# Optimization experiments

Measured on AMD Instinct MI355X. Metric: run time of the kernel, lower is better.

Reference implementation:

```python
import jax, jax.numpy as jnp
import numpy as np

N, E, F, H, DE, C, G = 50000, 800000, 128, 128, 16, 2, 32
NEG_SLOPE = 0.2

def setup_inputs() -> dict:
    key = jax.random.key(0)
    ks = jax.random.split(key, 13)
    s = 0.05  # small init scale for weights
    return {
        "x": jax.random.normal(ks[0], (N, F), jnp.float32),
        "edge_index": jax.random.randint(ks[1], (2, E), 0, N, dtype=jnp.int32),
        "edge_attr": jax.random.normal(ks[2], (E, DE), jnp.float32),
        "batch": jnp.sort(jax.random.randint(ks[3], (N,), 0, G, dtype=jnp.int32)),
        "Wl": jax.random.normal(ks[4], (F, H), jnp.float32) * s,
        "bl": jnp.zeros((H,), jnp.float32),
        "Wr": jax.random.normal(ks[5], (F, H), jnp.float32) * s,
        "br": jnp.zeros((H,), jnp.float32),
        "We": jax.random.normal(ks[6], (DE, H), jnp.float32) * s,
        "att": jax.random.normal(ks[7], (H,), jnp.float32) * s,
        "bias_conv": jnp.zeros((H,), jnp.float32),
        "Wc": jax.random.normal(ks[8], (H, C), jnp.float32) * s,
        "bc": jnp.zeros((C,), jnp.float32),
    }

def reference(x, edge_index, edge_attr, batch, Wl, bl, Wr, br, We, att, bias_conv, Wc, bc):
    n = x.shape[0]
    src, dst = edge_index[0], edge_index[1]
    # add self loops; self-loop edge_attr = mean of incoming edge_attr (PyG fill_value='mean')
    ones_e = jnp.ones((edge_attr.shape[0],), x.dtype)
    deg = jax.ops.segment_sum(ones_e, dst, num_segments=n)
    loop_attr = jax.ops.segment_sum(edge_attr, dst, num_segments=n) / jnp.maximum(deg, 1.0)[:, None]
    idx = jnp.arange(n, dtype=src.dtype)
    src2 = jnp.concatenate([src, idx])
    dst2 = jnp.concatenate([dst, idx])
    ea2 = jnp.concatenate([edge_attr, loop_attr], axis=0)  # [E+N, DE]
    # GATv2: separate source/target transforms
    xl = x @ Wl + bl          # [N, H] (source / message features)
    xr = x @ Wr + br          # [N, H] (target features)
    e = ea2 @ We              # [E+N, H]
    m = xl[src2] + xr[dst2] + e                      # per-edge features
    logit = jax.nn.leaky_relu(m, NEG_SLOPE) @ att    # [E+N]
    # segment softmax over destination nodes (every node has a self loop)
    mx = jax.ops.segment_max(logit, dst2, num_segments=n)
    ex = jnp.exp(logit - mx[dst2])
    den = jax.ops.segment_sum(ex, dst2, num_segments=n)
    alpha = ex / den[dst2]
    out = jax.ops.segment_sum(alpha[:, None] * xl[src2], dst2, num_segments=n) + bias_conv
    h = jax.nn.relu(out)
    # global mean pool over graphs (eval mode: dropout is identity)
    cnt = jax.ops.segment_sum(jnp.ones((n,), x.dtype), batch, num_segments=G)
    pooled = jax.ops.segment_sum(h, batch, num_segments=G) / jnp.maximum(cnt, 1.0)[:, None]
    return pooled @ Wc + bc
```

## Files before the change

### kernel.cpp

```cpp
#include <hip/hip_runtime.h>

#define FDIM 128
#define HDIM 128
#define DE   16
#define GG   32
#define CAP  64
#define NPB  4
#define EA_STRIDE 20
#define NEG_SLOPE 0.2f

__global__ void k_scatter(const int* __restrict__ src, const int* __restrict__ dst,
                          int* __restrict__ cursor, int2* __restrict__ list, int E) {
    int i = blockIdx.x * blockDim.x + threadIdx.x;
    if (i < E) {
        int d = dst[i];
        int p = atomicAdd(&cursor[d], 1);
        if (p < CAP - 1) list[d * CAP + p] = make_int2(src[i], i);
    }
}

__global__ __launch_bounds__(256) void k_gemm(
    const float* __restrict__ x,
    const float* __restrict__ Wl, const float* __restrict__ bl,
    const float* __restrict__ Wr, const float* __restrict__ br,
    float* __restrict__ xl, float* __restrict__ xr, int M)
{
    __shared__ float As[32][128];
    __shared__ float Bs[32][64];
    const int slab = blockIdx.y;
    const float* __restrict__ W    = (slab < 2) ? Wl : Wr;
    const float* __restrict__ bias = (slab < 2) ? bl : br;
    float* __restrict__ outp       = (slab < 2) ? xl : xr;
    const int cb = (slab & 1) * 64;
    const int r0 = blockIdx.x * 128;
    const int tid = threadIdx.x;
    const int tx = tid & 15, ty = tid >> 4;
    const int ma = ty * 4, mb = 64 + ty * 4, n0 = tx * 4;
    float acc[8][4] = {};

    for (int kc = 0; kc < FDIM; kc += 32) {
        #pragma unroll
        for (int vv = 0; vv < 4; ++vv) {
            int v = tid + vv * 256;
            int mrow = v >> 3, kq = v & 7;
            int r = r0 + mrow; r = (r < M) ? r : (M - 1);
            float4 xv = *reinterpret_cast<const float4*>(&x[(size_t)r * FDIM + kc + kq * 4]);
            As[kq * 4 + 0][mrow] = xv.x;
            As[kq * 4 + 1][mrow] = xv.y;
            As[kq * 4 + 2][mrow] = xv.z;
            As[kq * 4 + 3][mrow] = xv.w;
        }
        #pragma unroll
        for (int vv = 0; vv < 2; ++vv) {
            int v = tid + vv * 256;
            int k = v >> 4, nq = v & 15;
            *reinterpret_cast<float4*>(&Bs[k][nq * 4]) =
                *reinterpret_cast<const float4*>(&W[(size_t)(kc + k) * HDIM + cb + nq * 4]);
        }
        __syncthreads();
        #pragma unroll
        for (int k = 0; k < 32; ++k) {
            float4 b4 = *reinterpret_cast<const float4*>(&Bs[k][n0]);
            float4 aa = *reinterpret_cast<const float4*>(&As[k][ma]);
            float4 ab = *reinterpret_cast<const float4*>(&As[k][mb]);
            float a8[8] = {aa.x, aa.y, aa.z, aa.w, ab.x, ab.y, ab.z, ab.w};
            #pragma unroll
            for (int i = 0; i < 8; ++i) {
                acc[i][0] = fmaf(a8[i], b4.x, acc[i][0]);
                acc[i][1] = fmaf(a8[i], b4.y, acc[i][1]);
                acc[i][2] = fmaf(a8[i], b4.z, acc[i][2]);
                acc[i][3] = fmaf(a8[i], b4.w, acc[i][3]);
            }
        }
        __syncthreads();
    }
    float4 bv = *reinterpret_cast<const float4*>(&bias[cb + n0]);
    #pragma unroll
    for (int i = 0; i < 8; ++i) {
        int r = r0 + ((i < 4) ? (ma + i) : (mb + i - 4));
        if (r < M) {
            float4 o;
            o.x = acc[i][0] + bv.x; o.y = acc[i][1] + bv.y;
            o.z = acc[i][2] + bv.z; o.w = acc[i][3] + bv.w;
            *reinterpret_cast<float4*>(&outp[(size_t)r * HDIM + cb + n0]) = o;
        }
    }
}

__global__ __launch_bounds__(256, 4) void k_node(
    const float* __restrict__ xl, const float* __restrict__ xr,
    const float* __restrict__ edge_attr, const float* __restrict__ We,
    const float* __restrict__ att, const float* __restrict__ bias_conv,
    const int* __restrict__ deg, const int2* __restrict__ list,
    float* __restrict__ hN, int N)
{
    __shared__ float ea_s[NPB][CAP][EA_STRIDE];
    __shared__ int   srcs_s[NPB][CAP];
    __shared__ float T_s[NPB][8];

    const int tid  = threadIdx.x;
    const int lane = tid & 63;
    const int w    = tid >> 6;
    const int n    = blockIdx.x * NPB + w;
    if (n >= N) return;

    const float2 at2 = *reinterpret_cast<const float2*>(&att[2 * lane]);
    const float2 xr2 = *reinterpret_cast<const float2*>(&xr[(size_t)n * HDIM + 2 * lane]);
    float2 Wreg[DE];
    #pragma unroll
    for (int k = 0; k < DE; ++k)
        Wreg[k] = *reinterpret_cast<const float2*>(&We[k * HDIM + 2 * lane]);

    const int dfull  = deg[n];
    const int dcap   = dfull < (CAP - 1) ? dfull : (CAP - 1);
    const int cnt    = dcap + 1;
    const int nb     = (cnt + 7) >> 3;
    const int padcnt = nb * 8;

    if (lane < dcap) {
        int2 se = list[(size_t)n * CAP + lane];
        srcs_s[w][lane] = se.x;
        const float4* ep = reinterpret_cast<const float4*>(&edge_attr[(size_t)se.y * DE]);
        float4 v0 = ep[0], v1 = ep[1], v2 = ep[2], v3 = ep[3];
        float* row = &ea_s[w][lane][0];
        *reinterpret_cast<float4*>(row + 0)  = v0;
        *reinterpret_cast<float4*>(row + 4)  = v1;
        *reinterpret_cast<float4*>(row + 8)  = v2;
        *reinterpret_cast<float4*>(row + 12) = v3;
    } else if (lane < padcnt) {
        srcs_s[w][lane] = n;
    }
    asm volatile("s_waitcnt lgkmcnt(0)" ::: "memory");

    {
        const int k = lane & 15, q = lane >> 4;
        float s = 0.f;
        for (int j = q; j < dcap; j += 4) s += ea_s[w][j][k];
        s += __shfl_xor(s, 16);
        s += __shfl_xor(s, 32);
        if (q == 0) ea_s[w][dcap][k] = s / (float)(dfull > 1 ? dfull : 1);
    }
    asm volatile("s_waitcnt lgkmcnt(0)" ::: "memory");

    float m = -1e30f, d = 0.f, o0 = 0.f, o1 = 0.f;

    float2 A[8], B[8];
    int sA[8], sB[8];

    auto loadS = [&](int* s, int b) {
        const int4* p = reinterpret_cast<const int4*>(&srcs_s[w][b * 8]);
        int4 u0 = p[0], u1 = p[1];
        s[0] = u0.x; s[1] = u0.y; s[2] = u0.z; s[3] = u0.w;
        s[4] = u1.x; s[5] = u1.y; s[6] = u1.z; s[7] = u1.w;
    };
    auto issue = [&](float2* R, const int* s) {
        #pragma unroll
        for (int jj = 0; jj < 8; ++jj)
            R[jj] = *reinterpret_cast<const float2*>(&xl[(size_t)s[jj] * HDIM + 2 * lane]);
    };
    auto compute = [&](float2* R, int b) {
        const int j0 = b * 8;
        float p[8];
        #pragma unroll
        for (int jj = 0; jj < 8; ++jj) {
            const float* ear = &ea_s[w][j0 + jj][0];
            float4 e0 = *reinterpret_cast<const float4*>(ear + 0);
            float4 e1 = *reinterpret_cast<const float4*>(ear + 4);
            float4 e2 = *reinterpret_cast<const float4*>(ear + 8);
            float4 e3 = *reinterpret_cast<const float4*>(ear + 12);
            float s0 = xr2.x, s1 = xr2.y;
            s0 = fmaf(e0.x, Wreg[0].x,  s0); s1 = fmaf(e0.x, Wreg[0].y,  s1);
            s0 = fmaf(e0.y, Wreg[1].x,  s0); s1 = fmaf(e0.y, Wreg[1].y,  s1);
            s0 = fmaf(e0.z, Wreg[2].x,  s0); s1 = fmaf(e0.z, Wreg[2].y,  s1);
            s0 = fmaf(e0.w, Wreg[3].x,  s0); s1 = fmaf(e0.w, Wreg[3].y,  s1);
            s0 = fmaf(e1.x, Wreg[4].x,  s0); s1 = fmaf(e1.x, Wreg[4].y,  s1);
            s0 = fmaf(e1.y, Wreg[5].x,  s0); s1 = fmaf(e1.y, Wreg[5].y,  s1);
            s0 = fmaf(e1.z, Wreg[6].x,  s0); s1 = fmaf(e1.z, Wreg[6].y,  s1);
            s0 = fmaf(e1.w, Wreg[7].x,  s0); s1 = fmaf(e1.w, Wreg[7].y,  s1);
            s0 = fmaf(e2.x, Wreg[8].x,  s0); s1 = fmaf(e2.x, Wreg[8].y,  s1);
            s0 = fmaf(e2.y, Wreg[9].x,  s0); s1 = fmaf(e2.y, Wreg[9].y,  s1);
            s0 = fmaf(e2.z, Wreg[10].x, s0); s1 = fmaf(e2.z, Wreg[10].y, s1);
            s0 = fmaf(e2.w, Wreg[11].x, s0); s1 = fmaf(e2.w, Wreg[11].y, s1);
            s0 = fmaf(e3.x, Wreg[12].x, s0); s1 = fmaf(e3.x, Wreg[12].y, s1);
            s0 = fmaf(e3.y, Wreg[13].x, s0); s1 = fmaf(e3.y, Wreg[13].y, s1);
            s0 = fmaf(e3.z, Wreg[14].x, s0); s1 = fmaf(e3.z, Wreg[14].y, s1);
            s0 = fmaf(e3.w, Wreg[15].x, s0); s1 = fmaf(e3.w, Wreg[15].y, s1);
            s0 += R[jj].x;
            s1 += R[jj].y;
            s0 = s0 > 0.f ? s0 : NEG_SLOPE * s0;
            s1 = s1 > 0.f ? s1 : NEG_SLOPE * s1;
            p[jj] = fmaf(s0, at2.x, s1 * at2.y);
        }
        {
            float sd0 = (lane & 1) ? p[0] : p[4];
            float sd1 = (lane & 1) ? p[1] : p[5];
            float sd2 = (lane & 1) ? p[2] : p[6];
            float sd3 = (lane & 1) ? p[3] : p[7];
            float r0 = __shfl_xor(sd0, 1), r1 = __shfl_xor(sd1, 1);
            float r2 = __shfl_xor(sd2, 1), r3 = __shfl_xor(sd3, 1);
            p[0] = ((lane & 1) ? p[4] : p[0]) + r0;
            p[1] = ((lane & 1) ? p[5] : p[1]) + r1;
            p[2] = ((lane & 1) ? p[6] : p[2]) + r2;
            p[3] = ((lane & 1) ? p[7] : p[3]) + r3;
        }
        {
            float sd0 = (lane & 2) ? p[0] : p[2];
            float sd1 = (lane & 2) ? p[1] : p[3];
            float r0 = __shfl_xor(sd0, 2), r1 = __shfl_xor(sd1, 2);
            p[0] = ((lane & 2) ? p[2] : p[0]) + r0;
            p[1] = ((lane & 2) ? p[3] : p[1]) + r1;
        }
        {
            float sd = (lane & 4) ? p[0] : p[1];
            float r = __shfl_xor(sd, 4);
            p[0] = ((lane & 4) ? p[1] : p[0]) + r;
        }
        float t = p[0];
        t += __shfl_xor(t, 8);
        t += __shfl_xor(t, 16);
        t += __shfl_xor(t, 32);
        if (lane < 8) {
            int e = ((lane & 1) << 2) | (lane & 2) | ((lane >> 2) & 1);
            T_s[w][e] = t;
        }
        asm volatile("s_waitcnt lgkmcnt(0)" ::: "memory");
        float4 t0 = *reinterpret_cast<const float4*>(&T_s[w][0]);
        float4 t1 = *reinterpret_cast<const float4*>(&T_s[w][4]);
        float tt[8] = {t0.x, t0.y, t0.z, t0.w, t1.x, t1.y, t1.z, t1.w};

        const int bk = cnt - j0;
        float mx = m;
        #pragma unroll
        for (int jj = 0; jj < 8; ++jj) {
            if (jj >= bk) tt[jj] = -1e30f;
            mx = fmaxf(mx, tt[jj]);
        }
        const float sc = __expf(m - mx);
        float pj[8], psum = 0.f;
        #pragma unroll
        for (int jj = 0; jj < 8; ++jj) { pj[jj] = __expf(tt[jj] - mx); psum += pj[jj]; }
        d = fmaf(d, sc, psum);
        float acc0 = 0.f, acc1 = 0.f;
        #pragma unroll
        for (int jj = 0; jj < 8; ++jj) {
            acc0 = fmaf(pj[jj], R[jj].x, acc0);
            acc1 = fmaf(pj[jj], R[jj].y, acc1);
        }
        o0 = fmaf(o0, sc, acc0);
        o1 = fmaf(o1, sc, acc1);
        m = mx;
    };

    loadS(sA, 0); issue(A, sA);
    for (int b = 0; b < nb; ++b) {
        const bool odd = (b & 1) != 0;
        if (b + 1 < nb) {
            if (odd) { loadS(sA, b + 1); issue(A, sA); }
            else     { loadS(sB, b + 1); issue(B, sB); }
        }
        if (odd) compute(B, b); else compute(A, b);
    }

    const float inv = 1.f / d;
    const float2 bc2 = *reinterpret_cast<const float2*>(&bias_conv[2 * lane]);
    float2 res;
    res.x = fmaxf(fmaf(o0, inv, bc2.x), 0.f);
    res.y = fmaxf(fmaf(o1, inv, bc2.y), 0.f);
    *reinterpret_cast<float2*>(&hN[(size_t)n * HDIM + 2 * lane]) = res;
}

__global__ __launch_bounds__(128) void k_pool(
    const float* __restrict__ hN, const int* __restrict__ batch,
    float* __restrict__ pool, int* __restrict__ cnt, int N)
{
    const int t  = threadIdx.x;
    const int n0 = blockIdx.x * 256;
    if (n0 >= N) return;
    const int n1 = (n0 + 256 < N) ? (n0 + 256) : N;
    int curg = batch[n0];
    float acc = 0.f;
    int c = 0;
    for (int nn = n0; nn < n1; ++nn) {
        int g = batch[nn];
        if (g != curg) {
            atomicAdd(&pool[curg * HDIM + t], acc);
            if (t == 0) atomicAdd(&cnt[curg], c);
            acc = 0.f; c = 0; curg = g;
        }
        acc += hN[(size_t)nn * HDIM + t];
        ++c;
    }
    atomicAdd(&pool[curg * HDIM + t], acc);
    if (t == 0) atomicAdd(&cnt[curg], c);
}

__global__ void k_final(const float* __restrict__ pool, const int* __restrict__ cnt,
                        const float* __restrict__ Wc, const float* __restrict__ bc,
                        float* __restrict__ out)
{
    int t = threadIdx.x;
    if (t < GG * 2) {
        int g = t >> 1, c = t & 1;
        float inv = 1.f / (float)(cnt[g] > 1 ? cnt[g] : 1);
        float s = 0.f;
        #pragma unroll 16
        for (int h = 0; h < HDIM; ++h) s += pool[g * HDIM + h] * Wc[h * 2 + c];
        out[t] = s * inv + bc[c];
    }
}

extern "C" void kernel_launch(void* const* d_in, const int* in_sizes, int n_in,
                              void* d_out, int out_size, void* d_ws, size_t ws_size,
                              hipStream_t stream) {
    const float* x         = (const float*)d_in[0];
    const int*   ei        = (const int*)  d_in[1];
    const float* edge_attr = (const float*)d_in[2];
    const int*   batch     = (const int*)  d_in[3];
    const float* Wl        = (const float*)d_in[4];
    const float* bl        = (const float*)d_in[5];
    const float* Wr        = (const float*)d_in[6];
    const float* br        = (const float*)d_in[7];
    const float* We        = (const float*)d_in[8];
    const float* att       = (const float*)d_in[9];
    const float* bias_conv = (const float*)d_in[10];
    const float* Wc        = (const float*)d_in[11];
    const float* bc        = (const float*)d_in[12];
    float* out = (float*)d_out;

    const int N = in_sizes[0] / FDIM;
    const int E = in_sizes[1] / 2;
    const int* srcp = ei;
    const int* dstp = ei + E;

    char* ws = (char*)d_ws;
    size_t off = 0;
    auto alloc = [&](size_t bytes) { char* p = ws + off; off = (off + bytes + 255) & ~(size_t)255; return p; };
    int*   cursor = (int*)  alloc((size_t)N * 4);
    int2*  list   = (int2*) alloc((size_t)N * CAP * 8);
    float* xl     = (float*)alloc((size_t)N * HDIM * 4);
    float* xr     = (float*)alloc((size_t)N * HDIM * 4);
    float* hN     = (float*)alloc((size_t)N * HDIM * 4);
    float* pool   = (float*)alloc((size_t)GG * HDIM * 4);
    int*   cnt    = (int*)  alloc((size_t)GG * 4);

    hipMemsetAsync(cursor, 0, (size_t)N * 4, stream);
    hipMemsetAsync(pool,   0, (size_t)GG * HDIM * 4, stream);
    hipMemsetAsync(cnt,    0, (size_t)GG * 4, stream);

    k_scatter<<<(E + 255) / 256, 256, 0, stream>>>(srcp, dstp, cursor, list, E);
    k_gemm   <<<dim3((N + 127) / 128, 4), 256, 0, stream>>>(x, Wl, bl, Wr, br, xl, xr, N);
    k_node   <<<(N + NPB - 1) / NPB, 256, 0, stream>>>(xl, xr, edge_attr, We, att, bias_conv,
                                                       cursor, list, hN, N);
    k_pool   <<<(N + 255) / 256, 128, 0, stream>>>(hN, batch, pool, cnt, N);
    k_final  <<<1, 64, 0, stream>>>(pool, cnt, Wc, bc, out);
}
```

Measured before the change: 428.0 us.

## Fuse Wl/Wr GEMM tiles, fold pool zeroing, pack src ids in LDS, shrink pool chunks

The GEMM now computes both xl and xr in one 64-row tile with 8x8 per-thread accumulators. It also zeroes the pool and count buffers, which removes two memset launches and lets x be read once instead of four times. The node kernel stores source ids and softmax partials inside the padded edge-attr LDS rows and issues the first gather earlier, before the mean-loop computation. The pooling kernel uses smaller node chunks for more parallelism, at the cost of more atomics.

```diff
diff --git a/kernel.cpp b/kernel.cpp
--- a/kernel.cpp
+++ b/kernel.cpp
@@ -23,24 +23,25 @@
     const float* __restrict__ x,
     const float* __restrict__ Wl, const float* __restrict__ bl,
     const float* __restrict__ Wr, const float* __restrict__ br,
-    float* __restrict__ xl, float* __restrict__ xr, int M)
+    float* __restrict__ xl, float* __restrict__ xr, int M,
+    float* __restrict__ pool, int* __restrict__ cnt)
 {
-    __shared__ float As[32][128];
-    __shared__ float Bs[32][64];
-    const int slab = blockIdx.y;
-    const float* __restrict__ W    = (slab < 2) ? Wl : Wr;
-    const float* __restrict__ bias = (slab < 2) ? bl : br;
-    float* __restrict__ outp       = (slab < 2) ? xl : xr;
-    const int cb = (slab & 1) * 64;
-    const int r0 = blockIdx.x * 128;
+    __shared__ float As[32][65];
+    __shared__ float Bs[32][260];
+
     const int tid = threadIdx.x;
-    const int tx = tid & 15, ty = tid >> 4;
-    const int ma = ty * 4, mb = 64 + ty * 4, n0 = tx * 4;
-    float acc[8][4] = {};
+    if (blockIdx.x == 0) {
+        #pragma unroll
+        for (int i = tid; i < GG * HDIM; i += 256) pool[i] = 0.f;
+        if (tid < GG) cnt[tid] = 0;
+    }
+    const int r0 = blockIdx.x * 64;
+    const int tx = tid & 31, ty = tid >> 5;
+    float acc[8][8] = {};
 
     for (int kc = 0; kc < FDIM; kc += 32) {
         #pragma unroll
-        for (int vv = 0; vv < 4; ++vv) {
+        for (int vv = 0; vv < 2; ++vv) {
             int v = tid + vv * 256;
             int mrow = v >> 3, kq = v & 7;
             int r = r0 + mrow; r = (r < M) ? r : (M - 1);
@@ -51,38 +52,48 @@
             As[kq * 4 + 3][mrow] = xv.w;
         }
         #pragma unroll
-        for (int vv = 0; vv < 2; ++vv) {
+        for (int vv = 0; vv < 8; ++vv) {
             int v = tid + vv * 256;
-            int k = v >> 4, nq = v & 15;
-            *reinterpret_cast<float4*>(&Bs[k][nq * 4]) =
-                *reinterpret_cast<const float4*>(&W[(size_t)(kc + k) * HDIM + cb + nq * 4]);
+            int k = v >> 6, cq = v & 63;
+            const float* Wp = (cq < 32) ? &Wl[(size_t)(kc + k) * HDIM + cq * 4]
+                                        : &Wr[(size_t)(kc + k) * HDIM + (cq - 32) * 4];
+            *reinterpret_cast<float4*>(&Bs[k][cq * 4]) = *reinterpret_cast<const float4*>(Wp);
         }
         __syncthreads();
         #pragma unroll
         for (int k = 0; k < 32; ++k) {
-            float4 b4 = *reinterpret_cast<const float4*>(&Bs[k][n0]);
-            float4 aa = *reinterpret_cast<const float4*>(&As[k][ma]);
-            float4 ab = *reinterpret_cast<const float4*>(&As[k][mb]);
-            float a8[8] = {aa.x, aa.y, aa.z, aa.w, ab.x, ab.y, ab.z, ab.w};
+            float4 b0 = *reinterpret_cast<const float4*>(&Bs[k][tx * 4]);
+            float4 b1 = *reinterpret_cast<const float4*>(&Bs[k][128 + tx * 4]);
+            float4 a0 = *reinterpret_cast<const float4*>(&As[k][ty * 8]);
+            float4 a1 = *reinterpret_cast<const float4*>(&As[k][ty * 8 + 4]);
+            float a8[8] = {a0.x, a0.y, a0.z, a0.w, a1.x, a1.y, a1.z, a1.w};
             #pragma unroll
             for (int i = 0; i < 8; ++i) {
-                acc[i][0] = fmaf(a8[i], b4.x, acc[i][0]);
-                acc[i][1] = fmaf(a8[i], b4.y, acc[i][1]);
-                acc[i][2] = fmaf(a8[i], b4.z, acc[i][2]);
-                acc[i][3] = fmaf(a8[i], b4.w, acc[i][3]);
+                acc[i][0] = fmaf(a8[i], b0.x, acc[i][0]);
+                acc[i][1] = fmaf(a8[i], b0.y, acc[i][1]);
+                acc[i][2] = fmaf(a8[i], b0.z, acc[i][2]);
+                acc[i][3] = fmaf(a8[i], b0.w, acc[i][3]);
+                acc[i][4] = fmaf(a8[i], b1.x, acc[i][4]);
+                acc[i][5] = fmaf(a8[i], b1.y, acc[i][5]);
+                acc[i][6] = fmaf(a8[i], b1.z, acc[i][6]);
+                acc[i][7] = fmaf(a8[i], b1.w, acc[i][7]);
             }
         }
         __syncthreads();
     }
-    float4 bv = *reinterpret_cast<const float4*>(&bias[cb + n0]);
+    float4 bvl = *reinterpret_cast<const float4*>(&bl[tx * 4]);
+    float4 bvr = *reinterpret_cast<const float4*>(&br[tx * 4]);
     #pragma unroll
     for (int i = 0; i < 8; ++i) {
-        int r = r0 + ((i < 4) ? (ma + i) : (mb + i - 4));
+        int r = r0 + ty * 8 + i;
         if (r < M) {
-            float4 o;
-            o.x = acc[i][0] + bv.x; o.y = acc[i][1] + bv.y;
-            o.z = acc[i][2] + bv.z; o.w = acc[i][3] + bv.w;
-            *reinterpret_cast<float4*>(&outp[(size_t)r * HDIM + cb + n0]) = o;
+            float4 ol, orr;
+            ol.x  = acc[i][0] + bvl.x; ol.y  = acc[i][1] + bvl.y;
+            ol.z  = acc[i][2] + bvl.z; ol.w  = acc[i][3] + bvl.w;
+            orr.x = acc[i][4] + bvr.x; orr.y = acc[i][5] + bvr.y;
+            orr.z = acc[i][6] + bvr.z; orr.w = acc[i][7] + bvr.w;
+            *reinterpret_cast<float4*>(&xl[(size_t)r * HDIM + tx * 4]) = ol;
+            *reinterpret_cast<float4*>(&xr[(size_t)r * HDIM + tx * 4]) = orr;
         }
     }
 }
@@ -95,8 +106,6 @@
     float* __restrict__ hN, int N)
 {
     __shared__ float ea_s[NPB][CAP][EA_STRIDE];
-    __shared__ int   srcs_s[NPB][CAP];
-    __shared__ float T_s[NPB][8];
 
     const int tid  = threadIdx.x;
     const int lane = tid & 63;
@@ -119,7 +128,6 @@
 
     if (lane < dcap) {
         int2 se = list[(size_t)n * CAP + lane];
-        srcs_s[w][lane] = se.x;
         const float4* ep = reinterpret_cast<const float4*>(&edge_attr[(size_t)se.y * DE]);
         float4 v0 = ep[0], v1 = ep[1], v2 = ep[2], v3 = ep[3];
         float* row = &ea_s[w][lane][0];
@@ -127,10 +135,28 @@
         *reinterpret_cast<float4*>(row + 4)  = v1;
         *reinterpret_cast<float4*>(row + 8)  = v2;
         *reinterpret_cast<float4*>(row + 12) = v3;
+        row[16] = __int_as_float(se.x);
     } else if (lane < padcnt) {
-        srcs_s[w][lane] = n;
+        ea_s[w][lane][16] = __int_as_float(n);
     }
     asm volatile("s_waitcnt lgkmcnt(0)" ::: "memory");
+
+    float2 A[8], B[8];
+    int sA[8], sB[8];
+
+    auto loadS = [&](int* s, int b) {
+        #pragma unroll
+        for (int jj = 0; jj < 8; ++jj)
+            s[jj] = __float_as_int(ea_s[w][b * 8 + jj][16]);
+    };
+    auto issue = [&](float2* R, const int* s) {
+        #pragma unroll
+        for (int jj = 0; jj < 8; ++jj)
+            R[jj] = *reinterpret_cast<const float2*>(&xl[(size_t)s[jj] * HDIM + 2 * lane]);
+    };
+
+    loadS(sA, 0);
+    issue(A, sA);
 
     {
         const int k = lane & 15, q = lane >> 4;
@@ -144,20 +170,6 @@
 
     float m = -1e30f, d = 0.f, o0 = 0.f, o1 = 0.f;
 
-    float2 A[8], B[8];
-    int sA[8], sB[8];
-
-    auto loadS = [&](int* s, int b) {
-        const int4* p = reinterpret_cast<const int4*>(&srcs_s[w][b * 8]);
-        int4 u0 = p[0], u1 = p[1];
-        s[0] = u0.x; s[1] = u0.y; s[2] = u0.z; s[3] = u0.w;
-        s[4] = u1.x; s[5] = u1.y; s[6] = u1.z; s[7] = u1.w;
-    };
-    auto issue = [&](float2* R, const int* s) {
-        #pragma unroll
-        for (int jj = 0; jj < 8; ++jj)
-            R[jj] = *reinterpret_cast<const float2*>(&xl[(size_t)s[jj] * HDIM + 2 * lane]);
-    };
     auto compute = [&](float2* R, int b) {
         const int j0 = b * 8;
         float p[8];
@@ -221,12 +233,12 @@
         t += __shfl_xor(t, 32);
         if (lane < 8) {
             int e = ((lane & 1) << 2) | (lane & 2) | ((lane >> 2) & 1);
-            T_s[w][e] = t;
+            ea_s[w][e][17] = t;
         }
         asm volatile("s_waitcnt lgkmcnt(0)" ::: "memory");
-        float4 t0 = *reinterpret_cast<const float4*>(&T_s[w][0]);
-        float4 t1 = *reinterpret_cast<const float4*>(&T_s[w][4]);
-        float tt[8] = {t0.x, t0.y, t0.z, t0.w, t1.x, t1.y, t1.z, t1.w};
+        float tt[8];
+        #pragma unroll
+        for (int jj = 0; jj < 8; ++jj) tt[jj] = ea_s[w][jj][17];
 
         const int bk = cnt - j0;
         float mx = m;
@@ -251,7 +263,6 @@
         m = mx;
     };
 
-    loadS(sA, 0); issue(A, sA);
     for (int b = 0; b < nb; ++b) {
         const bool odd = (b & 1) != 0;
         if (b + 1 < nb) {
@@ -274,9 +285,9 @@
     float* __restrict__ pool, int* __restrict__ cnt, int N)
 {
     const int t  = threadIdx.x;
-    const int n0 = blockIdx.x * 256;
+    const int n0 = blockIdx.x * 64;
     if (n0 >= N) return;
-    const int n1 = (n0 + 256 < N) ? (n0 + 256) : N;
+    const int n1 = (n0 + 64 < N) ? (n0 + 64) : N;
     int curg = batch[n0];
     float acc = 0.f;
     int c = 0;
@@ -344,13 +355,11 @@
     int*   cnt    = (int*)  alloc((size_t)GG * 4);
 
     hipMemsetAsync(cursor, 0, (size_t)N * 4, stream);
-    hipMemsetAsync(pool,   0, (size_t)GG * HDIM * 4, stream);
-    hipMemsetAsync(cnt,    0, (size_t)GG * 4, stream);
 
     k_scatter<<<(E + 255) / 256, 256, 0, stream>>>(srcp, dstp, cursor, list, E);
-    k_gemm   <<<dim3((N + 127) / 128, 4), 256, 0, stream>>>(x, Wl, bl, Wr, br, xl, xr, N);
+    k_gemm   <<<(N + 63) / 64, 256, 0, stream>>>(x, Wl, bl, Wr, br, xl, xr, N, pool, cnt);
     k_node   <<<(N + NPB - 1) / NPB, 256, 0, stream>>>(xl, xr, edge_attr, We, att, bias_conv,
                                                        cursor, list, hN, N);
-    k_pool   <<<(N + 255) / 256, 128, 0, stream>>>(hN, batch, pool, cnt, N);
+    k_pool   <<<(N + 63) / 64, 128, 0, stream>>>(hN, batch, pool, cnt, N);
     k_final  <<<1, 64, 0, stream>>>(pool, cnt, Wc, bc, out);
 }
```

Measured after the change: 396.1 us. -7.5%, faster.
